# Kernel optimization log

Hardware: AMD Instinct MI355X
Metric: run time of the kernel (lower is better)

## Reference

```python
import jax, jax.numpy as jnp
import numpy as np
from jax import lax

N_NODES = 100000
N_EDGES = 1600000
DIM = 64
N_GRAPHS = 128
OUT = 10
BN_EPS = 1e-5


def setup_inputs() -> dict:
    key = jax.random.key(0)
    ks = jax.random.split(key, 8)
    s = 1.0 / np.sqrt(DIM)
    x = jax.random.normal(ks[0], (N_NODES, DIM), dtype=jnp.float32)
    edge_index = jax.random.randint(ks[1], (2, N_EDGES), 0, N_NODES, dtype=jnp.int64)
    batch = jnp.sort(jax.random.randint(ks[2], (N_NODES,), 0, N_GRAPHS, dtype=jnp.int64))
    return {
        "x": x,
        "edge_index": edge_index,
        "batch": batch,
        "W1": jax.random.normal(ks[3], (5, DIM, DIM), dtype=jnp.float32) * s,
        "b1": jnp.zeros((5, DIM), jnp.float32),
        "gamma": jnp.ones((5, DIM), jnp.float32),
        "beta": jnp.zeros((5, DIM), jnp.float32),
        "rmean": jnp.zeros((5, DIM), jnp.float32),
        "rvar": jnp.ones((5, DIM), jnp.float32),
        "W2": jax.random.normal(ks[4], (5, DIM, DIM), dtype=jnp.float32) * s,
        "b2": jnp.zeros((5, DIM), jnp.float32),
        "lin1_w": jax.random.normal(ks[5], (DIM, DIM), dtype=jnp.float32) * s,
        "lin1_b": jnp.zeros((DIM,), jnp.float32),
        "lin2_w": jax.random.normal(ks[6], (DIM, OUT), dtype=jnp.float32) * s,
        "lin2_b": jnp.zeros((OUT,), jnp.float32),
    }


def reference(x, edge_index, batch, W1, b1, gamma, beta, rmean, rvar, W2, b2,
              lin1_w, lin1_b, lin2_w, lin2_b):
    n = x.shape[0]
    src, dst = edge_index[0], edge_index[1]

    def gin_layer(h, p):
        w1, bb1, g, bt, m, v, w2, bb2 = p
        # GINConv (eps=0): h_i <- MLP(h_i + sum_{j in N(i)} h_j)
        agg = jax.ops.segment_sum(h[src], dst, num_segments=n)
        h = h + agg
        h = h @ w1 + bb1
        h = (h - m) * lax.rsqrt(v + BN_EPS) * g + bt  # BatchNorm1d (eval)
        h = jax.nn.relu(h)
        h = jax.nn.relu(h @ w2 + bb2)
        return h, None

    h, _ = lax.scan(gin_layer, x, (W1, b1, gamma, beta, rmean, rvar, W2, b2))
    # global_add_pool over graphs in the batch
    pooled = jax.ops.segment_sum(h, batch, num_segments=N_GRAPHS)  # [G, dim]
    pooled = jax.nn.relu(pooled @ lin1_w + lin1_b)
    # dropout is identity in eval mode
    return pooled @ lin2_w + lin2_b  # [G, out]
```

## Files before the change

kernel.cpp:

```cpp
#include <hip/hip_runtime.h>

#define N_NODES  100000
#define N_EDGES  1600000
#define DIM      64
#define N_GRAPHS 128
#define OUT_DIM  10
#define SCAN_NB    196
#define SCAN_CHUNK 512
#define RANGE_BITS 14
#define RANGE_SIZE 16384
#define N_RANGES   7
#define N_CHUNKS   32
#define CHUNK_EDGES (N_EDGES / N_CHUNKS)
#define NODE_PAD   (N_RANGES * RANGE_SIZE)

typedef unsigned int uint;
typedef unsigned short ushort;
typedef __attribute__((ext_vector_type(8))) short short8;
typedef __attribute__((ext_vector_type(4))) float f32x4;

__device__ __forceinline__ uint f2bf(float x) {
    uint b = __float_as_uint(x);
    b += 0x7fffu + ((b >> 16) & 1u);
    return b >> 16;
}


__global__ __launch_bounds__(1024) void histo_kernel(const int* __restrict__ dst,
                                                     int* __restrict__ counts8) {
    __shared__ int lds[RANGE_SIZE];
    const int c = blockIdx.x & (N_CHUNKS - 1);
    const int r = blockIdx.x >> 5;
    if (r >= N_RANGES) return;
    for (int j = threadIdx.x; j < RANGE_SIZE; j += 1024) lds[j] = 0;
    __syncthreads();
    const int beg = c * CHUNK_EDGES, end = beg + CHUNK_EDGES;
    for (int i0 = beg + threadIdx.x; i0 < end; i0 += 1024 * 8) {
        int d[8];
#pragma unroll
        for (int k = 0; k < 8; ++k) {
            const int i = i0 + k * 1024;
            d[k] = (i < end) ? dst[i] : -1;
        }
#pragma unroll
        for (int k = 0; k < 8; ++k)
            if ((d[k] >> RANGE_BITS) == r) atomicAdd(&lds[d[k] & (RANGE_SIZE - 1)], 1);
    }
    __syncthreads();
    int* outp = counts8 + (c * N_RANGES + r) * RANGE_SIZE;
    for (int j = threadIdx.x; j < RANGE_SIZE; j += 1024) outp[j] = lds[j];
}

__global__ void scanA_kernel(const int* __restrict__ counts8, int* __restrict__ blockSums, int n) {
    __shared__ int red[256];
    const int b = blockIdx.x, t = threadIdx.x;
    int s = 0;
#pragma unroll
    for (int k = 0; k < 2; ++k) {
        const int node = b * SCAN_CHUNK + t * 2 + k;
        if (node < n) {
            const int r = node >> RANGE_BITS, jj = node & (RANGE_SIZE - 1);
            for (int c = 0; c < N_CHUNKS; ++c)
                s += counts8[(c * N_RANGES + r) * RANGE_SIZE + jj];
        }
    }
    red[t] = s;
    __syncthreads();
    for (int off = 128; off > 0; off >>= 1) {
        if (t < off) red[t] += red[t + off];
        __syncthreads();
    }
    if (t == 0) blockSums[b] = red[0];
}

__global__ void scanB_kernel(const int* __restrict__ blockSums, int* __restrict__ blockOffs,
                             int* __restrict__ row_ptr) {
    __shared__ int sc[256];
    const int t = threadIdx.x;
    const int v = (t < SCAN_NB) ? blockSums[t] : 0;
    sc[t] = v;
    __syncthreads();
    for (int off = 1; off < 256; off <<= 1) {
        int u = (t >= off) ? sc[t - off] : 0;
        __syncthreads();
        sc[t] += u;
        __syncthreads();
    }
    if (t < SCAN_NB) blockOffs[t] = sc[t] - v;
    if (t == 255) row_ptr[N_NODES] = sc[255];
}

__global__ void scanC_kernel(const int* __restrict__ counts8, const int* __restrict__ blockOffs,
                             int* __restrict__ row_ptr, int* __restrict__ base8, int n) {
    __shared__ int sc[256];
    const int b = blockIdx.x, t = threadIdx.x;
    const int node0 = b * SCAN_CHUNK + t * 2;
    int cnt0[N_CHUNKS], cnt1[N_CHUNKS];
    int tot0 = 0, tot1 = 0;
    if (node0 < n) {
        const int r = node0 >> RANGE_BITS, jj = node0 & (RANGE_SIZE - 1);
        for (int c = 0; c < N_CHUNKS; ++c) {
            cnt0[c] = counts8[(c * N_RANGES + r) * RANGE_SIZE + jj];
            tot0 += cnt0[c];
        }
    }
    if (node0 + 1 < n) {
        const int r = (node0 + 1) >> RANGE_BITS, jj = (node0 + 1) & (RANGE_SIZE - 1);
        for (int c = 0; c < N_CHUNKS; ++c) {
            cnt1[c] = counts8[(c * N_RANGES + r) * RANGE_SIZE + jj];
            tot1 += cnt1[c];
        }
    }
    const int s = tot0 + tot1;
    sc[t] = s;
    __syncthreads();
    for (int off = 1; off < 256; off <<= 1) {
        int u = (t >= off) ? sc[t - off] : 0;
        __syncthreads();
        sc[t] += u;
        __syncthreads();
    }
    const int pre = blockOffs[b] + sc[t] - s;
    if (node0 < n) {
        row_ptr[node0] = pre;
        int run = pre;
        for (int c = 0; c < N_CHUNKS; ++c) { base8[c * NODE_PAD + node0] = run; run += cnt0[c]; }
    }
    if (node0 + 1 < n) {
        const int pre1 = pre + tot0;
        row_ptr[node0 + 1] = pre1;
        int run = pre1;
        for (int c = 0; c < N_CHUNKS; ++c) { base8[c * NODE_PAD + node0 + 1] = run; run += cnt1[c]; }
    }
}


__global__ __launch_bounds__(1024) void fill_kernel(const int* __restrict__ src,
                                                    const int* __restrict__ dst,
                                                    const int* __restrict__ base8,
                                                    int* __restrict__ col_idx) {
    __shared__ int lds[RANGE_SIZE];
    const int r = blockIdx.x & 7;
    const int c = blockIdx.x >> 3;
    if (r >= N_RANGES) return;
    const int* bp = base8 + c * NODE_PAD + r * RANGE_SIZE;
    for (int j = threadIdx.x; j < RANGE_SIZE; j += 1024)
        lds[j] = __builtin_nontemporal_load(&bp[j]);
    __syncthreads();
    const int beg = c * CHUNK_EDGES, end = beg + CHUNK_EDGES;
    for (int i0 = beg + threadIdx.x; i0 < end; i0 += 1024 * 8) {
        int d[8], s[8];
#pragma unroll
        for (int k = 0; k < 8; ++k) {
            const int i = i0 + k * 1024;
            d[k] = (i < end) ? __builtin_nontemporal_load(&dst[i]) : -1;
            s[k] = (i < end) ? __builtin_nontemporal_load(&src[i]) : 0;
        }
#pragma unroll
        for (int k = 0; k < 8; ++k) {
            if ((d[k] >> RANGE_BITS) == r) {
                int pos = atomicAdd(&lds[d[k] & (RANGE_SIZE - 1)], 1);
                col_idx[pos] = s[k];
            }
        }
    }
}


__global__ void cvt_kernel(const float* __restrict__ x, ushort* __restrict__ xb, int n4) {
    int idx = blockIdx.x * blockDim.x + threadIdx.x;
    if (idx >= n4) return;
    float4 v = ((const float4*)x)[idx];
    uint2 o;
    o.x = f2bf(v.x) | (f2bf(v.y) << 16);
    o.y = f2bf(v.z) | (f2bf(v.w) << 16);
    ((uint2*)xb)[idx] = o;
}


__global__ void repack_kernel(const float* __restrict__ W1, const float* __restrict__ W2,
                              uint4* __restrict__ Wp) {
    const int wave = (blockIdx.x * blockDim.x + threadIdx.x) >> 6;
    if (wave >= 10) return;
    const int layer = wave >> 1;
    const float* W = (wave & 1) ? (W2 + layer * 4096) : (W1 + layer * 4096);
    const int lane = threadIdx.x & 63;
    const int n15 = lane & 15, quad = lane >> 4;
#pragma unroll
    for (int f = 0; f < 8; ++f) {
        const int outer = f >> 1, h = f & 1;
        uint p[4];
#pragma unroll
        for (int pj = 0; pj < 4; ++pj) {
            const int k0 = h * 32 + quad * 8 + 2 * pj;
            uint lo = f2bf(W[k0 * 64 + outer * 16 + n15]);
            uint hi = f2bf(W[(k0 + 1) * 64 + outer * 16 + n15]);
            p[pj] = lo | (hi << 16);
        }
        Wp[(wave * 8 + f) * 64 + lane] = make_uint4(p[0], p[1], p[2], p[3]);
    }
}


__device__ __forceinline__ void add_unpack(float acc[8], uint4 v) {
    acc[0] += __uint_as_float(v.x << 16);
    acc[1] += __uint_as_float(v.x & 0xffff0000u);
    acc[2] += __uint_as_float(v.y << 16);
    acc[3] += __uint_as_float(v.y & 0xffff0000u);
    acc[4] += __uint_as_float(v.z << 16);
    acc[5] += __uint_as_float(v.z & 0xffff0000u);
    acc[6] += __uint_as_float(v.w << 16);
    acc[7] += __uint_as_float(v.w & 0xffff0000u);
}

__global__ __launch_bounds__(256) void agg_kernel(
    const ushort* __restrict__ hb, ushort* __restrict__ tb,
    const int* __restrict__ row_ptr, const int* __restrict__ col_idx, int n)
{
    const uint4* __restrict__ hb4 = (const uint4*)hb;
    const int lane = threadIdx.x & 63;
    const int g = lane >> 3;
    const int q = lane & 7;
    const int wave = (blockIdx.x * blockDim.x + threadIdx.x) >> 6;
    const int i = wave * 8 + g;
    if (i >= n) return;
    const int rp0 = row_ptr[i];
    const int deg = row_ptr[i + 1] - rp0;

    float acc[8];
    {
        uint4 v = hb4[(size_t)i * 8 + q];
        acc[0] = __uint_as_float(v.x << 16);
        acc[1] = __uint_as_float(v.x & 0xffff0000u);
        acc[2] = __uint_as_float(v.y << 16);
        acc[3] = __uint_as_float(v.y & 0xffff0000u);
        acc[4] = __uint_as_float(v.z << 16);
        acc[5] = __uint_as_float(v.z & 0xffff0000u);
        acc[6] = __uint_as_float(v.w << 16);
        acc[7] = __uint_as_float(v.w & 0xffff0000u);
    }

    int e = 0;
    for (; e + 8 <= deg; e += 8) {
        int ix[8];
#pragma unroll
        for (int k = 0; k < 8; ++k) ix[k] = col_idx[rp0 + e + k];
        uint4 v[8];
#pragma unroll
        for (int k = 0; k < 8; ++k) v[k] = hb4[(size_t)ix[k] * 8 + q];
#pragma unroll
        for (int k = 0; k < 8; ++k) add_unpack(acc, v[k]);
    }
    if (e + 4 <= deg) {
        int ix[4];
#pragma unroll
        for (int k = 0; k < 4; ++k) ix[k] = col_idx[rp0 + e + k];
        uint4 v[4];
#pragma unroll
        for (int k = 0; k < 4; ++k) v[k] = hb4[(size_t)ix[k] * 8 + q];
#pragma unroll
        for (int k = 0; k < 4; ++k) add_unpack(acc, v[k]);
        e += 4;
    }
    for (; e < deg; ++e) {
        int ix = col_idx[rp0 + e];
        uint4 v = hb4[(size_t)ix * 8 + q];
        add_unpack(acc, v);
    }

    uint4 o;
    o.x = f2bf(acc[0]) | (f2bf(acc[1]) << 16);
    o.y = f2bf(acc[2]) | (f2bf(acc[3]) << 16);
    o.z = f2bf(acc[4]) | (f2bf(acc[5]) << 16);
    o.w = f2bf(acc[6]) | (f2bf(acc[7]) << 16);
    ((uint4*)tb)[(size_t)i * 8 + q] = o;
}


__global__ __launch_bounds__(256) void mlp_kernel(
    const ushort* __restrict__ tb, ushort* __restrict__ hb,
    const uint4* __restrict__ Wp,
    const float* __restrict__ b1, const float* __restrict__ gamma,
    const float* __restrict__ beta, const float* __restrict__ rmean,
    const float* __restrict__ rvar, const float* __restrict__ b2, int ntiles)
{
    __shared__ __align__(16) ushort U[4][16][72];
    const int lane = threadIdx.x & 63;
    const int wid  = threadIdx.x >> 6;
    const int n15  = lane & 15, quad = lane >> 4;

    short8 w1f[8], w2f[8];
    const short8* Wp8 = (const short8*)Wp;
#pragma unroll
    for (int f = 0; f < 8; ++f) {
        w1f[f] = Wp8[f * 64 + lane];
        w2f[f] = Wp8[(8 + f) * 64 + lane];
    }
    f32x4 sc[4], sh[4];
#pragma unroll
    for (int mt = 0; mt < 4; ++mt) {
        const int j0 = mt * 16 + quad * 4;
#pragma unroll
        for (int r = 0; r < 4; ++r) {
            float s = gamma[j0 + r] * rsqrtf(rvar[j0 + r] + 1e-5f);
            sc[mt][r] = s;
            sh[mt][r] = (b1[j0 + r] - rmean[j0 + r]) * s + beta[j0 + r];
        }
    }
    float bb2[4];
#pragma unroll
    for (int tc = 0; tc < 4; ++tc) bb2[tc] = b2[tc * 16 + n15];

    const int wave = blockIdx.x * 4 + wid;
    const int nwaves = gridDim.x * 4;
    for (int tile = wave; tile < ntiles; tile += nwaves) {
        const int nb = tile * 16;
        const short8* trow = (const short8*)(tb + (size_t)(nb + n15) * 64);
        short8 t0 = trow[quad];
        short8 t1 = trow[4 + quad];

        f32x4 c1[4];
#pragma unroll
        for (int mt = 0; mt < 4; ++mt) {
            c1[mt] = (f32x4){0.f, 0.f, 0.f, 0.f};
            c1[mt] = __builtin_amdgcn_mfma_f32_16x16x32_bf16(w1f[mt * 2 + 0], t0, c1[mt], 0, 0, 0);
            c1[mt] = __builtin_amdgcn_mfma_f32_16x16x32_bf16(w1f[mt * 2 + 1], t1, c1[mt], 0, 0, 0);
        }
#pragma unroll
        for (int mt = 0; mt < 4; ++mt) {
            float u0 = fmaxf(c1[mt][0] * sc[mt][0] + sh[mt][0], 0.f);
            float u1 = fmaxf(c1[mt][1] * sc[mt][1] + sh[mt][1], 0.f);
            float u2 = fmaxf(c1[mt][2] * sc[mt][2] + sh[mt][2], 0.f);
            float u3 = fmaxf(c1[mt][3] * sc[mt][3] + sh[mt][3], 0.f);
            uint2 pk;
            pk.x = f2bf(u0) | (f2bf(u1) << 16);
            pk.y = f2bf(u2) | (f2bf(u3) << 16);
            *(uint2*)&U[wid][n15][mt * 16 + quad * 4] = pk;
        }
        __threadfence_block();
        short8 u0 = *(const short8*)&U[wid][n15][quad * 8];
        short8 u1 = *(const short8*)&U[wid][n15][32 + quad * 8];

        f32x4 c2[4];
#pragma unroll
        for (int tc = 0; tc < 4; ++tc) {
            c2[tc] = (f32x4){0.f, 0.f, 0.f, 0.f};
            c2[tc] = __builtin_amdgcn_mfma_f32_16x16x32_bf16(u0, w2f[tc * 2 + 0], c2[tc], 0, 0, 0);
            c2[tc] = __builtin_amdgcn_mfma_f32_16x16x32_bf16(u1, w2f[tc * 2 + 1], c2[tc], 0, 0, 0);
        }
#pragma unroll
        for (int tc = 0; tc < 4; ++tc) {
#pragma unroll
            for (int r = 0; r < 4; ++r) {
                float v = fmaxf(c2[tc][r] + bb2[tc], 0.f);
                hb[(size_t)(nb + quad * 4 + r) * 64 + tc * 16 + n15] = (ushort)f2bf(v);
            }
        }
    }
}


__global__ void pool_kernel(const ushort* __restrict__ hb, const int* __restrict__ batch,
                            float* __restrict__ pooled, int n) {
    const int lane = threadIdx.x & 63;
    const int wid  = threadIdx.x >> 6;
    const int wave = blockIdx.x * 4 + wid;
    const int nwaves = gridDim.x * 4;
    const int per = (n + nwaves - 1) / nwaves;
    const int a = wave * per;
    const int b = min(a + per, n);
    if (a >= b) return;
    int cur = batch[a];
    float sum = 0.0f;
    for (int i = a; i < b; ++i) {
        int g = batch[i];
        if (g != cur) {
            atomicAdd(&pooled[cur * DIM + lane], sum);
            sum = 0.0f;
            cur = g;
        }
        sum += __uint_as_float(((uint)hb[(size_t)i * DIM + lane]) << 16);
    }
    atomicAdd(&pooled[cur * DIM + lane], sum);
}


__global__ void head_kernel(const float* __restrict__ pooled,
                            const float* __restrict__ w1, const float* __restrict__ b1,
                            const float* __restrict__ w2, const float* __restrict__ b2,
                            float* __restrict__ out) {
    const int g = blockIdx.x;
    const int lane = threadIdx.x;
    __shared__ float pl[DIM];
    __shared__ float y1l[DIM];
    pl[lane] = pooled[g * DIM + lane];
    __syncthreads();
    float y = b1[lane];
#pragma unroll
    for (int d = 0; d < DIM; ++d) y += pl[d] * w1[d * DIM + lane];
    y1l[lane] = fmaxf(y, 0.0f);
    __syncthreads();
    if (lane < OUT_DIM) {
        float y2 = b2[lane];
#pragma unroll
        for (int d = 0; d < DIM; ++d) y2 += y1l[d] * w2[d * OUT_DIM + lane];
        out[g * OUT_DIM + lane] = y2;
    }
}


extern "C" void kernel_launch(void* const* d_in, const int* in_sizes, int n_in,
                              void* d_out, int out_size, void* d_ws, size_t ws_size,
                              hipStream_t stream) {
    const float* x     = (const float*)d_in[0];
    const int*   eidx  = (const int*)  d_in[1];
    const int*   batch = (const int*)  d_in[2];
    const float* W1    = (const float*)d_in[3];
    const float* b1    = (const float*)d_in[4];
    const float* gamma = (const float*)d_in[5];
    const float* beta  = (const float*)d_in[6];
    const float* rmean = (const float*)d_in[7];
    const float* rvar  = (const float*)d_in[8];
    const float* W2    = (const float*)d_in[9];
    const float* b2    = (const float*)d_in[10];
    const float* l1w   = (const float*)d_in[11];
    const float* l1b   = (const float*)d_in[12];
    const float* l2w   = (const float*)d_in[13];
    const float* l2b   = (const float*)d_in[14];
    float* out = (float*)d_out;

    const size_t C8 = (size_t)N_CHUNKS * N_RANGES * RANGE_SIZE;
    const size_t B8 = (size_t)N_CHUNKS * NODE_PAD;
    int* counts8   = (int*)d_ws;
    int* row_ptr   = counts8   + C8;
    int* blockSums = row_ptr   + 100352;
    int* blockOffs = blockSums + 256;
    int* base8     = blockOffs + 256;
    int* col_idx   = base8     + B8;
    uint4* Wp      = (uint4*)(col_idx + 1600000);
    ushort* tb     = (ushort*)(Wp + 5120);
    ushort* hb     = tb + (size_t)N_NODES * DIM;
    float* pooled  = (float*)(hb + (size_t)N_NODES * DIM);

    const int* srcp = eidx;
    const int* dstp = eidx + N_EDGES;

    hipMemsetAsync(pooled, 0, N_GRAPHS * DIM * sizeof(float), stream);

    cvt_kernel<<<(N_NODES * DIM / 4 + 255) / 256, 256, 0, stream>>>(x, hb, N_NODES * DIM / 4);
    repack_kernel<<<1, 640, 0, stream>>>(W1, W2, Wp);
    histo_kernel<<<N_CHUNKS * 8, 1024, 0, stream>>>(dstp, counts8);
    scanA_kernel<<<SCAN_NB, 256, 0, stream>>>(counts8, blockSums, N_NODES);
    scanB_kernel<<<1, 256, 0, stream>>>(blockSums, blockOffs, row_ptr);
    scanC_kernel<<<SCAN_NB, 256, 0, stream>>>(counts8, blockOffs, row_ptr, base8, N_NODES);
    fill_kernel<<<N_CHUNKS * 8, 1024, 0, stream>>>(srcp, dstp, base8, col_idx);

    const int agg_blocks = ((N_NODES + 7) / 8 * 64 + 255) / 256;
    const int ntiles = N_NODES / 16;

    for (int l = 0; l < 5; ++l) {
        agg_kernel<<<agg_blocks, 256, 0, stream>>>(hb, tb, row_ptr, col_idx, N_NODES);
        mlp_kernel<<<512, 256, 0, stream>>>(
            tb, hb, Wp + (size_t)l * 2 * 8 * 64,
            b1 + (size_t)l * DIM, gamma + (size_t)l * DIM, beta + (size_t)l * DIM,
            rmean + (size_t)l * DIM, rvar + (size_t)l * DIM, b2 + (size_t)l * DIM, ntiles);
    }
    pool_kernel<<<2048, 256, 0, stream>>>(hb, batch, pooled, N_NODES);
    head_kernel<<<N_GRAPHS, 64, 0, stream>>>(pooled, l1w, l1b, l2w, l2b, out);
}
```

Before: 405.9 us.

## Fuse neighbor aggregation and MLP into one per-layer kernel with ping-pong buffers

Merges agg_kernel and mlp_kernel into a single layer_kernel. Each wave gathers and sums neighbors for its 16-node tile into LDS, then runs both MFMA matmuls and writes to a ping-pong output buffer. This removes the global round-trip of the aggregated tensor and halves the launches per layer. The cost is lower gather parallelism per wave (two sequential row passes), block-wide syncthreads in the tile loop, and weights reloaded from memory on every tile. It also drops the nontemporal loads in fill_kernel.

```diff
diff --git a/kernel.cpp b/kernel.cpp
--- a/kernel.cpp
+++ b/kernel.cpp
@@ -153,8 +153,8 @@
 #pragma unroll
         for (int k = 0; k < 8; ++k) {
             const int i = i0 + k * 1024;
-            d[k] = (i < end) ? __builtin_nontemporal_load(&dst[i]) : -1;
-            s[k] = (i < end) ? __builtin_nontemporal_load(&src[i]) : 0;
+            d[k] = (i < end) ? dst[i] : -1;
+            s[k] = (i < end) ? src[i] : 0;
         }
 #pragma unroll
         for (int k = 0; k < 8; ++k) {
@@ -213,89 +213,24 @@
     acc[7] += __uint_as_float(v.w & 0xffff0000u);
 }
 
-__global__ __launch_bounds__(256) void agg_kernel(
-    const ushort* __restrict__ hb, ushort* __restrict__ tb,
-    const int* __restrict__ row_ptr, const int* __restrict__ col_idx, int n)
-{
-    const uint4* __restrict__ hb4 = (const uint4*)hb;
-    const int lane = threadIdx.x & 63;
-    const int g = lane >> 3;
-    const int q = lane & 7;
-    const int wave = (blockIdx.x * blockDim.x + threadIdx.x) >> 6;
-    const int i = wave * 8 + g;
-    if (i >= n) return;
-    const int rp0 = row_ptr[i];
-    const int deg = row_ptr[i + 1] - rp0;
-
-    float acc[8];
-    {
-        uint4 v = hb4[(size_t)i * 8 + q];
-        acc[0] = __uint_as_float(v.x << 16);
-        acc[1] = __uint_as_float(v.x & 0xffff0000u);
-        acc[2] = __uint_as_float(v.y << 16);
-        acc[3] = __uint_as_float(v.y & 0xffff0000u);
-        acc[4] = __uint_as_float(v.z << 16);
-        acc[5] = __uint_as_float(v.z & 0xffff0000u);
-        acc[6] = __uint_as_float(v.w << 16);
-        acc[7] = __uint_as_float(v.w & 0xffff0000u);
-    }
-
-    int e = 0;
-    for (; e + 8 <= deg; e += 8) {
-        int ix[8];
-#pragma unroll
-        for (int k = 0; k < 8; ++k) ix[k] = col_idx[rp0 + e + k];
-        uint4 v[8];
-#pragma unroll
-        for (int k = 0; k < 8; ++k) v[k] = hb4[(size_t)ix[k] * 8 + q];
-#pragma unroll
-        for (int k = 0; k < 8; ++k) add_unpack(acc, v[k]);
-    }
-    if (e + 4 <= deg) {
-        int ix[4];
-#pragma unroll
-        for (int k = 0; k < 4; ++k) ix[k] = col_idx[rp0 + e + k];
-        uint4 v[4];
-#pragma unroll
-        for (int k = 0; k < 4; ++k) v[k] = hb4[(size_t)ix[k] * 8 + q];
-#pragma unroll
-        for (int k = 0; k < 4; ++k) add_unpack(acc, v[k]);
-        e += 4;
-    }
-    for (; e < deg; ++e) {
-        int ix = col_idx[rp0 + e];
-        uint4 v = hb4[(size_t)ix * 8 + q];
-        add_unpack(acc, v);
-    }
-
-    uint4 o;
-    o.x = f2bf(acc[0]) | (f2bf(acc[1]) << 16);
-    o.y = f2bf(acc[2]) | (f2bf(acc[3]) << 16);
-    o.z = f2bf(acc[4]) | (f2bf(acc[5]) << 16);
-    o.w = f2bf(acc[6]) | (f2bf(acc[7]) << 16);
-    ((uint4*)tb)[(size_t)i * 8 + q] = o;
-}
-
-
-__global__ __launch_bounds__(256) void mlp_kernel(
-    const ushort* __restrict__ tb, ushort* __restrict__ hb,
+__global__ __launch_bounds__(256) void layer_kernel(
+    const ushort* __restrict__ hbp, ushort* __restrict__ hbn,
+    const int* __restrict__ row_ptr, const int* __restrict__ col_idx,
     const uint4* __restrict__ Wp,
     const float* __restrict__ b1, const float* __restrict__ gamma,
     const float* __restrict__ beta, const float* __restrict__ rmean,
     const float* __restrict__ rvar, const float* __restrict__ b2, int ntiles)
 {
-    __shared__ __align__(16) ushort U[4][16][72];
+    __shared__ __align__(16) ushort Ua[4][16][72];
+    __shared__ __align__(16) ushort Ub[4][16][72];
+    const uint4* __restrict__ hb4 = (const uint4*)hbp;
     const int lane = threadIdx.x & 63;
     const int wid  = threadIdx.x >> 6;
     const int n15  = lane & 15, quad = lane >> 4;
-
-    short8 w1f[8], w2f[8];
+    const int g = lane >> 3;
+    const int q = lane & 7;
     const short8* Wp8 = (const short8*)Wp;
-#pragma unroll
-    for (int f = 0; f < 8; ++f) {
-        w1f[f] = Wp8[f * 64 + lane];
-        w2f[f] = Wp8[(8 + f) * 64 + lane];
-    }
+
     f32x4 sc[4], sh[4];
 #pragma unroll
     for (int mt = 0; mt < 4; ++mt) {
@@ -311,49 +246,114 @@
 #pragma unroll
     for (int tc = 0; tc < 4; ++tc) bb2[tc] = b2[tc * 16 + n15];
 
-    const int wave = blockIdx.x * 4 + wid;
     const int nwaves = gridDim.x * 4;
-    for (int tile = wave; tile < ntiles; tile += nwaves) {
+    for (int tbase = blockIdx.x * 4; tbase < ntiles; tbase += nwaves) {
+        const int tile = tbase + wid;
+        const bool active = tile < ntiles;
         const int nb = tile * 16;
-        const short8* trow = (const short8*)(tb + (size_t)(nb + n15) * 64);
-        short8 t0 = trow[quad];
-        short8 t1 = trow[4 + quad];
-
-        f32x4 c1[4];
-#pragma unroll
-        for (int mt = 0; mt < 4; ++mt) {
-            c1[mt] = (f32x4){0.f, 0.f, 0.f, 0.f};
-            c1[mt] = __builtin_amdgcn_mfma_f32_16x16x32_bf16(w1f[mt * 2 + 0], t0, c1[mt], 0, 0, 0);
-            c1[mt] = __builtin_amdgcn_mfma_f32_16x16x32_bf16(w1f[mt * 2 + 1], t1, c1[mt], 0, 0, 0);
-        }
-#pragma unroll
-        for (int mt = 0; mt < 4; ++mt) {
-            float u0 = fmaxf(c1[mt][0] * sc[mt][0] + sh[mt][0], 0.f);
-            float u1 = fmaxf(c1[mt][1] * sc[mt][1] + sh[mt][1], 0.f);
-            float u2 = fmaxf(c1[mt][2] * sc[mt][2] + sh[mt][2], 0.f);
-            float u3 = fmaxf(c1[mt][3] * sc[mt][3] + sh[mt][3], 0.f);
-            uint2 pk;
-            pk.x = f2bf(u0) | (f2bf(u1) << 16);
-            pk.y = f2bf(u2) | (f2bf(u3) << 16);
-            *(uint2*)&U[wid][n15][mt * 16 + quad * 4] = pk;
-        }
-        __threadfence_block();
-        short8 u0 = *(const short8*)&U[wid][n15][quad * 8];
-        short8 u1 = *(const short8*)&U[wid][n15][32 + quad * 8];
-
-        f32x4 c2[4];
-#pragma unroll
-        for (int tc = 0; tc < 4; ++tc) {
-            c2[tc] = (f32x4){0.f, 0.f, 0.f, 0.f};
-            c2[tc] = __builtin_amdgcn_mfma_f32_16x16x32_bf16(u0, w2f[tc * 2 + 0], c2[tc], 0, 0, 0);
-            c2[tc] = __builtin_amdgcn_mfma_f32_16x16x32_bf16(u1, w2f[tc * 2 + 1], c2[tc], 0, 0, 0);
-        }
-#pragma unroll
-        for (int tc = 0; tc < 4; ++tc) {
-#pragma unroll
-            for (int r = 0; r < 4; ++r) {
-                float v = fmaxf(c2[tc][r] + bb2[tc], 0.f);
-                hb[(size_t)(nb + quad * 4 + r) * 64 + tc * 16 + n15] = (ushort)f2bf(v);
+
+        if (active) {
+            for (int ro = 0; ro < 2; ++ro) {
+                const int i = nb + ro * 8 + g;
+                const int rp0 = row_ptr[i];
+                const int deg = row_ptr[i + 1] - rp0;
+                float acc[8];
+                {
+                    uint4 v = hb4[(size_t)i * 8 + q];
+                    acc[0] = __uint_as_float(v.x << 16);
+                    acc[1] = __uint_as_float(v.x & 0xffff0000u);
+                    acc[2] = __uint_as_float(v.y << 16);
+                    acc[3] = __uint_as_float(v.y & 0xffff0000u);
+                    acc[4] = __uint_as_float(v.z << 16);
+                    acc[5] = __uint_as_float(v.z & 0xffff0000u);
+                    acc[6] = __uint_as_float(v.w << 16);
+                    acc[7] = __uint_as_float(v.w & 0xffff0000u);
+                }
+                int e = 0;
+                for (; e + 8 <= deg; e += 8) {
+                    int ix[8];
+#pragma unroll
+                    for (int k = 0; k < 8; ++k) ix[k] = col_idx[rp0 + e + k];
+                    uint4 v[8];
+#pragma unroll
+                    for (int k = 0; k < 8; ++k) v[k] = hb4[(size_t)ix[k] * 8 + q];
+#pragma unroll
+                    for (int k = 0; k < 8; ++k) add_unpack(acc, v[k]);
+                }
+                if (e + 4 <= deg) {
+                    int ix[4];
+#pragma unroll
+                    for (int k = 0; k < 4; ++k) ix[k] = col_idx[rp0 + e + k];
+                    uint4 v[4];
+#pragma unroll
+                    for (int k = 0; k < 4; ++k) v[k] = hb4[(size_t)ix[k] * 8 + q];
+#pragma unroll
+                    for (int k = 0; k < 4; ++k) add_unpack(acc, v[k]);
+                    e += 4;
+                }
+                for (; e < deg; ++e) {
+                    int ix = col_idx[rp0 + e];
+                    uint4 v = hb4[(size_t)ix * 8 + q];
+                    add_unpack(acc, v);
+                }
+                uint2 o0, o1;
+                o0.x = f2bf(acc[0]) | (f2bf(acc[1]) << 16);
+                o0.y = f2bf(acc[2]) | (f2bf(acc[3]) << 16);
+                o1.x = f2bf(acc[4]) | (f2bf(acc[5]) << 16);
+                o1.y = f2bf(acc[6]) | (f2bf(acc[7]) << 16);
+                *(uint2*)&Ua[wid][ro * 8 + g][q * 8]     = o0;
+                *(uint2*)&Ua[wid][ro * 8 + g][q * 8 + 4] = o1;
+            }
+        }
+        __syncthreads();
+
+        if (active) {
+            short8 t0 = *(const short8*)&Ua[wid][n15][quad * 8];
+            short8 t1 = *(const short8*)&Ua[wid][n15][32 + quad * 8];
+            short8 wf[8];
+#pragma unroll
+            for (int f = 0; f < 8; ++f) wf[f] = Wp8[f * 64 + lane];
+            f32x4 c1[4];
+#pragma unroll
+            for (int mt = 0; mt < 4; ++mt) {
+                c1[mt] = (f32x4){0.f, 0.f, 0.f, 0.f};
+                c1[mt] = __builtin_amdgcn_mfma_f32_16x16x32_bf16(wf[mt * 2 + 0], t0, c1[mt], 0, 0, 0);
+                c1[mt] = __builtin_amdgcn_mfma_f32_16x16x32_bf16(wf[mt * 2 + 1], t1, c1[mt], 0, 0, 0);
+            }
+#pragma unroll
+            for (int mt = 0; mt < 4; ++mt) {
+                float u0 = fmaxf(c1[mt][0] * sc[mt][0] + sh[mt][0], 0.f);
+                float u1 = fmaxf(c1[mt][1] * sc[mt][1] + sh[mt][1], 0.f);
+                float u2 = fmaxf(c1[mt][2] * sc[mt][2] + sh[mt][2], 0.f);
+                float u3 = fmaxf(c1[mt][3] * sc[mt][3] + sh[mt][3], 0.f);
+                uint2 pk;
+                pk.x = f2bf(u0) | (f2bf(u1) << 16);
+                pk.y = f2bf(u2) | (f2bf(u3) << 16);
+                *(uint2*)&Ub[wid][n15][mt * 16 + quad * 4] = pk;
+            }
+        }
+        __syncthreads();
+
+        if (active) {
+            short8 u0 = *(const short8*)&Ub[wid][n15][quad * 8];
+            short8 u1 = *(const short8*)&Ub[wid][n15][32 + quad * 8];
+            short8 wf[8];
+#pragma unroll
+            for (int f = 0; f < 8; ++f) wf[f] = Wp8[(8 + f) * 64 + lane];
+            f32x4 c2[4];
+#pragma unroll
+            for (int tc = 0; tc < 4; ++tc) {
+                c2[tc] = (f32x4){0.f, 0.f, 0.f, 0.f};
+                c2[tc] = __builtin_amdgcn_mfma_f32_16x16x32_bf16(u0, wf[tc * 2 + 0], c2[tc], 0, 0, 0);
+                c2[tc] = __builtin_amdgcn_mfma_f32_16x16x32_bf16(u1, wf[tc * 2 + 1], c2[tc], 0, 0, 0);
+            }
+#pragma unroll
+            for (int tc = 0; tc < 4; ++tc) {
+#pragma unroll
+                for (int r = 0; r < 4; ++r) {
+                    float v = fmaxf(c2[tc][r] + bb2[tc], 0.f);
+                    hbn[(size_t)(nb + quad * 4 + r) * 64 + tc * 16 + n15] = (ushort)f2bf(v);
+                }
             }
         }
     }
@@ -455,16 +455,16 @@
     scanC_kernel<<<SCAN_NB, 256, 0, stream>>>(counts8, blockOffs, row_ptr, base8, N_NODES);
     fill_kernel<<<N_CHUNKS * 8, 1024, 0, stream>>>(srcp, dstp, base8, col_idx);
 
-    const int agg_blocks = ((N_NODES + 7) / 8 * 64 + 255) / 256;
     const int ntiles = N_NODES / 16;
-
+    ushort* cur = hb;
+    ushort* nxt = tb;
     for (int l = 0; l < 5; ++l) {
-        agg_kernel<<<agg_blocks, 256, 0, stream>>>(hb, tb, row_ptr, col_idx, N_NODES);
-        mlp_kernel<<<512, 256, 0, stream>>>(
-            tb, hb, Wp + (size_t)l * 2 * 8 * 64,
+        layer_kernel<<<782, 256, 0, stream>>>(
+            cur, nxt, row_ptr, col_idx, Wp + (size_t)l * 2 * 8 * 64,
             b1 + (size_t)l * DIM, gamma + (size_t)l * DIM, beta + (size_t)l * DIM,
             rmean + (size_t)l * DIM, rvar + (size_t)l * DIM, b2 + (size_t)l * DIM, ntiles);
-    }
-    pool_kernel<<<2048, 256, 0, stream>>>(hb, batch, pooled, N_NODES);
+        ushort* t = cur; cur = nxt; nxt = t;
+    }
+    pool_kernel<<<2048, 256, 0, stream>>>(cur, batch, pooled, N_NODES);
     head_kernel<<<N_GRAPHS, 64, 0, stream>>>(pooled, l1w, l1b, l2w, l2b, out);
 }
```

Result: slower. 451.0 us (+11.1%).
